# Performance work log

Hardware: AMD Instinct MI355X
Metric: run time of the kernel (lower is better)

The kernel has to match this reference:

```python
import jax, jax.numpy as jnp
import numpy as np

N_NODES = 100000
N_EDGES = 3200000
EMBED_DIM = 64
BATCH = 16384


def setup_inputs() -> dict:
    key = jax.random.key(0)
    k1, k2, k3, k4 = jax.random.split(key, 4)
    gcn_weight = jax.random.normal(k1, (N_NODES, EMBED_DIM), dtype=jnp.float32) * 0.1
    gcn_bias = jnp.zeros((EMBED_DIM,), dtype=jnp.float32)
    linear_weight = jax.random.normal(k2, (N_NODES, 1), dtype=jnp.float32) * 0.1
    linear_bias = jnp.zeros((1,), dtype=jnp.float32)
    edge_index = jax.random.randint(k3, (2, N_EDGES), 0, N_NODES, dtype=jnp.int64)
    interaction_pairs = jax.random.randint(k4, (BATCH, 2), 0, N_NODES, dtype=jnp.int64)
    return {
        "gcn_weight": gcn_weight,
        "gcn_bias": gcn_bias,
        "linear_weight": linear_weight,
        "linear_bias": linear_bias,
        "edge_index": edge_index,
        "interaction_pairs": interaction_pairs,
    }


def _gcn_conv_identity_features(gcn_weight, gcn_bias, edge_index):
    # Features X = I, so X @ W = W. GCNConv output = D^{-1/2}(A+I)D^{-1/2} W + b.
    src, dst = edge_index[0], edge_index[1]
    ones = jnp.ones((src.shape[0],), dtype=gcn_weight.dtype)
    # degree (with self loop) computed on destination nodes, as in PyG gcn_norm
    deg = jax.ops.segment_sum(ones, dst, num_segments=N_NODES) + 1.0
    dinv = jax.lax.rsqrt(deg)  # [N]
    norm = dinv[src] * dinv[dst]  # [E]
    msg = gcn_weight[src] * norm[:, None]  # [E, D] -- dominant memory traffic
    agg = jax.ops.segment_sum(msg, dst, num_segments=N_NODES)  # [N, D]
    # self-loop term: norm_ii = 1/deg[i]
    out = agg + gcn_weight * (dinv * dinv)[:, None] + gcn_bias
    return out


def reference(gcn_weight, gcn_bias, linear_weight, linear_bias, edge_index, interaction_pairs):
    node_emb = _gcn_conv_identity_features(gcn_weight, gcn_bias, edge_index)  # [N, D]
    e = node_emb[interaction_pairs]  # [B, 2, D] gather
    # FM pairwise interaction: 0.5 * sum_d ((sum_f e)^2 - sum_f e^2)
    sum_sq = jnp.square(jnp.sum(e, axis=1))  # [B, D]
    sq_sum = jnp.sum(jnp.square(e), axis=1)  # [B, D]
    fm = 0.5 * jnp.sum(sum_sq - sq_sum, axis=1, keepdims=True)  # [B, 1]
    # FeaturesLinear: sum of per-node scalar embeddings + bias
    lin = jnp.sum(linear_weight[interaction_pairs], axis=1) + linear_bias  # [B, 1]
    return jnp.squeeze(lin + fm, axis=1)  # [B]
```

## Files before the change

kernel.cpp:

```cpp
#include <hip/hip_runtime.h>

#define N_NODES 100000
#define N_EDGES 3200000
#define BATCH 16384
#define MAX_SLOTS 32768
#define MAGIC 0x5A5A5A5Au

#define NW 12500
#define SLICES 256
#define EPS2 12500
#define I4PS2 3125

#define NBUCK 256
#define BSH 7

#define OFF_SLOT      0
#define OFF_COUNTERS  400000
#define OFF_DINV      400064
#define OFF_NODELIST  800064
#define OFF_BTOT      931136
#define OFF_BPART     932160
#define OFF_SLOTSTART 1194304
#define OFF_PARTIALS  1325440
#define OFF_WH        14125440
#define OFF_BINS      26925440
#define OFF_BINS2     31725440
#define OFF_EMB       36525440

__device__ __forceinline__ unsigned bfr(float f) {
    unsigned u = __float_as_uint(f);
    return (u + 0x7FFFu + ((u >> 16) & 1u)) >> 16;
}
__device__ __forceinline__ float bfx(unsigned h) {
    return __uint_as_float(h << 16);
}

__global__ void k_flags(const int* __restrict__ pairs, unsigned* __restrict__ slot,
                        int* __restrict__ counters) {
    int i = blockIdx.x * blockDim.x + threadIdx.x;
    if (i < 16) counters[i] = 0;
    if (i < 2 * BATCH) slot[pairs[i]] = MAGIC;
}

__global__ void k_compact(unsigned* __restrict__ slot, int* __restrict__ nodelist,
                          int* __restrict__ counters) {
    int n = blockIdx.x * blockDim.x + threadIdx.x;
    int lane = threadIdx.x & 63;
    int want = (n < N_NODES && slot[n] == MAGIC) ? 1 : 0;
    int incl = want;
#pragma unroll
    for (int d = 1; d < 64; d <<= 1) {
        int t = __shfl_up(incl, d, 64);
        if (lane >= d) incl += t;
    }
    int total = __shfl(incl, 63, 64);
    int base = 0;
    if (lane == 63 && total > 0) base = atomicAdd(&counters[0], total);
    base = __shfl(base, 63, 64);
    if (n < N_NODES) {
        if (want) {
            int s = base + incl - 1;
            slot[n] = (unsigned)(s + 1);
            nodelist[s] = n;
        } else {
            slot[n] = 0u;
        }
    }
}

__device__ __forceinline__ void hist1n(int d, unsigned* h) {
    atomicAdd(&h[d >> 3], 1u << ((d & 7) << 2));
}

__global__ void k_hist(const int* __restrict__ dst, const unsigned* __restrict__ slot,
                       unsigned* __restrict__ partials, int* __restrict__ bpart) {
    __shared__ unsigned h[NW];
    __shared__ int lc[NBUCK];
    int g = blockIdx.x;
    for (int i = threadIdx.x; i < NW; i += 512) h[i] = 0;
    if (threadIdx.x < NBUCK) lc[threadIdx.x] = 0;
    __syncthreads();
    const int4* d4 = (const int4*)(dst + g * EPS2);
    for (int i = threadIdx.x; i < I4PS2; i += 512) {
        int4 v = d4[i];
        hist1n(v.x, h); hist1n(v.y, h); hist1n(v.z, h); hist1n(v.w, h);
        unsigned r;
        r = slot[v.x]; if (r) atomicAdd(&lc[(r - 1) >> BSH], 1);
        r = slot[v.y]; if (r) atomicAdd(&lc[(r - 1) >> BSH], 1);
        r = slot[v.z]; if (r) atomicAdd(&lc[(r - 1) >> BSH], 1);
        r = slot[v.w]; if (r) atomicAdd(&lc[(r - 1) >> BSH], 1);
    }
    __syncthreads();
    unsigned* outp = partials + (unsigned)g * NW;
    for (int i = threadIdx.x; i < NW; i += 512) outp[i] = h[i];
    if (threadIdx.x < NBUCK) bpart[threadIdx.x * SLICES + g] = lc[threadIdx.x];
}

__global__ void k_mid(const unsigned* __restrict__ partials, const float4* __restrict__ w4,
                      float* __restrict__ dinv, uint4* __restrict__ wh4,
                      int* __restrict__ bpart, int* __restrict__ btot) {
    if (blockIdx.x >= 391) {
        __shared__ int t[SLICES];
        int b = blockIdx.x - 391, g = threadIdx.x;
        int v = bpart[b * SLICES + g];
        t[g] = v;
        __syncthreads();
        for (int off = 1; off < SLICES; off <<= 1) {
            int x = (g >= off) ? t[g - off] : 0;
            __syncthreads();
            t[g] += x;
            __syncthreads();
        }
        bpart[b * SLICES + g] = t[g] - v;
        if (g == SLICES - 1) btot[b] = t[g];
        return;
    }
    __shared__ unsigned pA[256], pB[256], pC[256], pD[256];
    __shared__ float sdinv[256];
    int blk = blockIdx.x;
    int wi = threadIdx.x & 31, sg = threadIdx.x >> 5;
    int w = blk * 32 + wi;
    unsigned A = 0, B = 0, C = 0, D = 0;
    if (w < NW) {
        const unsigned* q = partials + w;
#pragma unroll
        for (int ch = 0; ch < 2; ++ch) {
            unsigned x = 0, y = 0;
#pragma unroll
            for (int k = 0; k < 16; ++k) {
                unsigned v = q[(unsigned)(sg * 32 + ch * 16 + k) * NW];
                x += v & 0x0F0F0F0Fu;
                y += (v >> 4) & 0x0F0F0F0Fu;
            }
            A += x & 0x00FF00FFu;
            B += (x >> 8) & 0x00FF00FFu;
            C += y & 0x00FF00FFu;
            D += (y >> 8) & 0x00FF00FFu;
        }
    }
    pA[threadIdx.x] = A; pB[threadIdx.x] = B; pC[threadIdx.x] = C; pD[threadIdx.x] = D;
    __syncthreads();
    if (threadIdx.x < 32 && w < NW) {
        unsigned sA = 0, sB = 0, sC = 0, sD = 0;
#pragma unroll
        for (int k = 0; k < 8; ++k) {
            sA += pA[k * 32 + wi]; sB += pB[k * 32 + wi];
            sC += pC[k * 32 + wi]; sD += pD[k * 32 + wi];
        }
        float4 d0, d1;
        d0.x = rsqrtf((float)(sA & 0xFFFFu) + 1.0f);
        d0.y = rsqrtf((float)(sC & 0xFFFFu) + 1.0f);
        d0.z = rsqrtf((float)(sB & 0xFFFFu) + 1.0f);
        d0.w = rsqrtf((float)(sD & 0xFFFFu) + 1.0f);
        d1.x = rsqrtf((float)(sA >> 16) + 1.0f);
        d1.y = rsqrtf((float)(sC >> 16) + 1.0f);
        d1.z = rsqrtf((float)(sB >> 16) + 1.0f);
        d1.w = rsqrtf((float)(sD >> 16) + 1.0f);
        ((float4*)dinv)[w * 2] = d0;
        ((float4*)dinv)[w * 2 + 1] = d1;
        int lb = wi * 8;
        sdinv[lb + 0] = d0.x; sdinv[lb + 1] = d0.y; sdinv[lb + 2] = d0.z; sdinv[lb + 3] = d0.w;
        sdinv[lb + 4] = d1.x; sdinv[lb + 5] = d1.y; sdinv[lb + 6] = d1.z; sdinv[lb + 7] = d1.w;
    }
    __syncthreads();
#pragma unroll
    for (int it = 0; it < 8; ++it) {
        int k = blk * 2048 + it * 256 + threadIdx.x;
        if (k < N_NODES * 8) {
            float4 va = w4[k * 2];
            float4 vb = w4[k * 2 + 1];
            float d = sdinv[(k >> 3) - blk * 256];
            uint4 o;
            o.x = bfr(va.x * d) | (bfr(va.y * d) << 16);
            o.y = bfr(va.z * d) | (bfr(va.w * d) << 16);
            o.z = bfr(vb.x * d) | (bfr(vb.y * d) << 16);
            o.w = bfr(vb.z * d) | (bfr(vb.w * d) << 16);
            wh4[k] = o;
        }
    }
}

__device__ __forceinline__ void scat1(int d, int s, const unsigned* __restrict__ slot,
                                      int* cur, int* __restrict__ bins) {
    unsigned r = slot[d];
    if (r) {
        int sl = (int)r - 1;
        int pos = atomicAdd(&cur[sl >> BSH], 1);
        bins[pos] = ((sl & 127) << 17) | s;
    }
}

__global__ void k_bscatter(const int* __restrict__ src, const int* __restrict__ dst,
                           const unsigned* __restrict__ slot, const int* __restrict__ bpart,
                           const int* __restrict__ btot, int* __restrict__ bins) {
    __shared__ int tb[NBUCK], vv[NBUCK], cur[NBUCK];
    int g = blockIdx.x;
    int t = threadIdx.x;
    if (t < NBUCK) { int v = btot[t]; vv[t] = v; tb[t] = v; }
    __syncthreads();
    for (int off = 1; off < NBUCK; off <<= 1) {
        int x = (t < NBUCK && t >= off) ? tb[t - off] : 0;
        __syncthreads();
        if (t < NBUCK) tb[t] += x;
        __syncthreads();
    }
    if (t < NBUCK) cur[t] = tb[t] - vv[t] + bpart[t * SLICES + g];
    __syncthreads();
    const int4* d4 = (const int4*)(dst + g * EPS2);
    const int4* s4 = (const int4*)(src + g * EPS2);
    for (int i = t; i < I4PS2; i += 512) {
        int4 d = d4[i];
        int4 s = s4[i];
        scat1(d.x, s.x, slot, cur, bins);
        scat1(d.y, s.y, slot, cur, bins);
        scat1(d.z, s.z, slot, cur, bins);
        scat1(d.w, s.w, slot, cur, bins);
    }
}

__global__ void k_bsort(const int* __restrict__ btot, const int* __restrict__ bins,
                        int* __restrict__ slotstart, int* __restrict__ bins2) {
    __shared__ int tb[NBUCK], vv[NBUCK];
    __shared__ int lc[128], st[128];
    int b = blockIdx.x;
    int tid = threadIdx.x;
    { int v = btot[tid]; vv[tid] = v; tb[tid] = v; }
    __syncthreads();
    for (int off = 1; off < NBUCK; off <<= 1) {
        int x = (tid >= off) ? tb[tid - off] : 0;
        __syncthreads();
        tb[tid] += x;
        __syncthreads();
    }
    int beg = tb[b] - vv[b];
    int end = beg + vv[b];
    if (tid < 128) lc[tid] = 0;
    __syncthreads();
    for (int j = beg + tid; j < end; j += 256)
        atomicAdd(&lc[(bins[j] >> 17) & 127], 1);
    __syncthreads();
    if (tid < 128) st[tid] = lc[tid];
    __syncthreads();
    for (int off = 1; off < 128; off <<= 1) {
        int v = (tid < 128 && tid >= off) ? st[tid - off] : 0;
        __syncthreads();
        if (tid < 128) st[tid] += v;
        __syncthreads();
    }
    if (tid < 128) {
        int s0 = beg + st[tid] - lc[tid];
        slotstart[(b << 7) + tid] = s0;
        lc[tid] = s0;
    }
    if (b == NBUCK - 1 && tid == 0) slotstart[MAX_SLOTS] = tb[NBUCK - 1];
    __syncthreads();
    for (int j = beg + tid; j < end; j += 256) {
        int e = bins[j];
        int pos = atomicAdd(&lc[(e >> 17) & 127], 1);
        bins2[pos] = e & 0x1FFFF;
    }
}

__global__ void k_gather(const int* __restrict__ nodelist, const int* __restrict__ slotstart,
                         const int* __restrict__ bins2, const uint4* __restrict__ wh4,
                         const float* __restrict__ dinv, const float4* __restrict__ bias4,
                         const int* __restrict__ counters, uint4* __restrict__ emb4) {
    int s = (blockIdx.x * blockDim.x + threadIdx.x) >> 6;
    int lane = threadIdx.x & 63;
    if (s >= counters[0]) return;
    int rg = lane >> 3, dp = lane & 7;
    int beg = slotstart[s], end = slotstart[s + 1];
    float a0 = 0.f, a1 = 0.f, a2 = 0.f, a3 = 0.f, a4 = 0.f, a5 = 0.f, a6 = 0.f, a7 = 0.f;
    int j = beg;
    for (; j + 16 <= end; j += 16) {
        int e0 = bins2[j + rg];
        int e1 = bins2[j + 8 + rg];
        uint4 oa = wh4[(e0 << 3) + dp];
        uint4 ob = wh4[(e1 << 3) + dp];
        a0 += bfx(oa.x) + bfx(ob.x);
        a1 += bfx(oa.x >> 16) + bfx(ob.x >> 16);
        a2 += bfx(oa.y) + bfx(ob.y);
        a3 += bfx(oa.y >> 16) + bfx(ob.y >> 16);
        a4 += bfx(oa.z) + bfx(ob.z);
        a5 += bfx(oa.z >> 16) + bfx(ob.z >> 16);
        a6 += bfx(oa.w) + bfx(ob.w);
        a7 += bfx(oa.w >> 16) + bfx(ob.w >> 16);
    }
    for (; j < end; j += 8) {
        if (rg < end - j) {
            int e0 = bins2[j + rg];
            uint4 oa = wh4[(e0 << 3) + dp];
            a0 += bfx(oa.x); a1 += bfx(oa.x >> 16);
            a2 += bfx(oa.y); a3 += bfx(oa.y >> 16);
            a4 += bfx(oa.z); a5 += bfx(oa.z >> 16);
            a6 += bfx(oa.w); a7 += bfx(oa.w >> 16);
        }
    }
#pragma unroll
    for (int m = 8; m <= 32; m <<= 1) {
        a0 += __shfl_xor(a0, m, 64); a1 += __shfl_xor(a1, m, 64);
        a2 += __shfl_xor(a2, m, 64); a3 += __shfl_xor(a3, m, 64);
        a4 += __shfl_xor(a4, m, 64); a5 += __shfl_xor(a5, m, 64);
        a6 += __shfl_xor(a6, m, 64); a7 += __shfl_xor(a7, m, 64);
    }
    if (rg == 0) {
        int n = nodelist[s];
        float dn = dinv[n];
        uint4 u = wh4[(n << 3) + dp];
        float4 b0 = bias4[dp * 2], b1 = bias4[dp * 2 + 1];
        float r0 = (a0 + bfx(u.x)) * dn + b0.x;
        float r1 = (a1 + bfx(u.x >> 16)) * dn + b0.y;
        float r2 = (a2 + bfx(u.y)) * dn + b0.z;
        float r3 = (a3 + bfx(u.y >> 16)) * dn + b0.w;
        float r4 = (a4 + bfx(u.z)) * dn + b1.x;
        float r5 = (a5 + bfx(u.z >> 16)) * dn + b1.y;
        float r6 = (a6 + bfx(u.w)) * dn + b1.z;
        float r7 = (a7 + bfx(u.w >> 16)) * dn + b1.w;
        uint4 o;
        o.x = bfr(r0) | (bfr(r1) << 16);
        o.y = bfr(r2) | (bfr(r3) << 16);
        o.z = bfr(r4) | (bfr(r5) << 16);
        o.w = bfr(r6) | (bfr(r7) << 16);
        emb4[(s << 3) + dp] = o;
    }
}

__global__ void k_final(const int* __restrict__ pairs, const unsigned* __restrict__ slot,
                        const uint2* __restrict__ emb2, const float* __restrict__ lw,
                        const float* __restrict__ lb, float* __restrict__ out) {
    int p = (blockIdx.x * blockDim.x + threadIdx.x) >> 4;
    int li = threadIdx.x & 15;
    if (p >= BATCH) return;
    int a = pairs[p * 2], b = pairs[p * 2 + 1];
    int sa = (int)slot[a] - 1;
    int sb = (int)slot[b] - 1;
    uint2 ua = emb2[(sa << 4) + li];
    uint2 ub = emb2[(sb << 4) + li];
    float prod = bfx(ua.x) * bfx(ub.x) + bfx(ua.x >> 16) * bfx(ub.x >> 16)
               + bfx(ua.y) * bfx(ub.y) + bfx(ua.y >> 16) * bfx(ub.y >> 16);
#pragma unroll
    for (int m = 1; m <= 8; m <<= 1) prod += __shfl_xor(prod, m, 64);
    if (li == 0) out[p] = lw[a] + lw[b] + lb[0] + prod;
}

extern "C" void kernel_launch(void* const* d_in, const int* in_sizes, int n_in,
                              void* d_out, int out_size, void* d_ws, size_t ws_size,
                              hipStream_t stream) {
    const float* gcn_weight    = (const float*)d_in[0];
    const float* gcn_bias      = (const float*)d_in[1];
    const float* linear_weight = (const float*)d_in[2];
    const float* linear_bias   = (const float*)d_in[3];
    const int*   edge_index    = (const int*)d_in[4];
    const int*   pairs         = (const int*)d_in[5];
    float* out = (float*)d_out;

    char* ws = (char*)d_ws;
    unsigned* slot      = (unsigned*)(ws + OFF_SLOT);
    int*      counters  = (int*)     (ws + OFF_COUNTERS);
    float*    dinv      = (float*)   (ws + OFF_DINV);
    int*      nodelist  = (int*)     (ws + OFF_NODELIST);
    int*      btot      = (int*)     (ws + OFF_BTOT);
    int*      bpart     = (int*)     (ws + OFF_BPART);
    int*      slotstart = (int*)     (ws + OFF_SLOTSTART);
    unsigned* partials  = (unsigned*)(ws + OFF_PARTIALS);
    uint4*    wh4       = (uint4*)   (ws + OFF_WH);
    int*      bins      = (int*)     (ws + OFF_BINS);
    int*      bins2     = (int*)     (ws + OFF_BINS2);
    uint4*    emb4      = (uint4*)   (ws + OFF_EMB);
    uint2*    emb2      = (uint2*)   (ws + OFF_EMB);

    const int* src_arr = edge_index;
    const int* dst_arr = edge_index + N_EDGES;

    k_flags<<<128, 256, 0, stream>>>(pairs, slot, counters);
    k_compact<<<391, 256, 0, stream>>>(slot, nodelist, counters);
    k_hist<<<SLICES, 512, 0, stream>>>(dst_arr, slot, partials, bpart);
    k_mid<<<391 + 256, 256, 0, stream>>>(partials, (const float4*)gcn_weight, dinv, wh4,
                                         bpart, btot);
    k_bscatter<<<SLICES, 512, 0, stream>>>(src_arr, dst_arr, slot, bpart, btot, bins);
    k_bsort<<<NBUCK, 256, 0, stream>>>(btot, bins, slotstart, bins2);
    k_gather<<<MAX_SLOTS / 4, 256, 0, stream>>>(nodelist, slotstart, bins2, wh4,
                                                dinv, (const float4*)gcn_bias,
                                                counters, emb4);
    k_final<<<1024, 256, 0, stream>>>(pairs, slot, emb2, linear_weight, linear_bias, out);
}
```

Baseline: 198.0 us.

## Fuse pipeline stages into one persistent kernel with software grid barriers

Replaces seven separate kernel launches with a single persistent 512-block kernel that runs compaction, histogram, dinv/bf16 conversion, prefix scans, bucket scatter, bucket sort, gather and final FM stages, separated by atomic-counter grid barriers. The bucket-partial granularity is doubled to 512 sub-slices so every block participates in the scatter phase. The aim is to remove per-launch overhead and inter-kernel gaps. In exchange it adds spin-wait barrier costs and depends on all 512 blocks being co-resident, which risks deadlock if occupancy is lower than assumed.

```diff
diff --git a/kernel.cpp b/kernel.cpp
--- a/kernel.cpp
+++ b/kernel.cpp
@@ -6,11 +6,12 @@
 #define MAX_SLOTS 32768
 #define MAGIC 0x5A5A5A5Au
 
+#define GRID 512
+#define TPB 512
+
 #define NW 12500
-#define SLICES 256
-#define EPS2 12500
-#define I4PS2 3125
-
+#define HSLICES 256
+#define NSUB 512
 #define NBUCK 256
 #define BSH 7
 
@@ -20,12 +21,12 @@
 #define OFF_NODELIST  800064
 #define OFF_BTOT      931136
 #define OFF_BPART     932160
-#define OFF_SLOTSTART 1194304
-#define OFF_PARTIALS  1325440
-#define OFF_WH        14125440
-#define OFF_BINS      26925440
-#define OFF_BINS2     31725440
-#define OFF_EMB       36525440
+#define OFF_SLOTSTART 1456448
+#define OFF_PARTIALS  1587584
+#define OFF_WH        14387584
+#define OFF_BINS      27187584
+#define OFF_BINS2     31987584
+#define OFF_EMB       36787584
 
 __device__ __forceinline__ unsigned bfr(float f) {
     unsigned u = __float_as_uint(f);
@@ -35,326 +36,29 @@
     return __uint_as_float(h << 16);
 }
 
-__global__ void k_flags(const int* __restrict__ pairs, unsigned* __restrict__ slot,
+__device__ __forceinline__ void gbar(int* cnt, int target) {
+    __syncthreads();
+    if (threadIdx.x == 0) {
+        __threadfence();
+        atomicAdd(cnt, 1);
+        while (atomicAdd(cnt, 0) < target) __builtin_amdgcn_s_sleep(8);
+        __threadfence();
+    }
+    __syncthreads();
+}
+
+__global__ void k_init0(const int* __restrict__ pairs, unsigned* __restrict__ slot,
                         int* __restrict__ counters) {
     int i = blockIdx.x * blockDim.x + threadIdx.x;
     if (i < 16) counters[i] = 0;
     if (i < 2 * BATCH) slot[pairs[i]] = MAGIC;
 }
 
-__global__ void k_compact(unsigned* __restrict__ slot, int* __restrict__ nodelist,
-                          int* __restrict__ counters) {
-    int n = blockIdx.x * blockDim.x + threadIdx.x;
-    int lane = threadIdx.x & 63;
-    int want = (n < N_NODES && slot[n] == MAGIC) ? 1 : 0;
-    int incl = want;
-#pragma unroll
-    for (int d = 1; d < 64; d <<= 1) {
-        int t = __shfl_up(incl, d, 64);
-        if (lane >= d) incl += t;
-    }
-    int total = __shfl(incl, 63, 64);
-    int base = 0;
-    if (lane == 63 && total > 0) base = atomicAdd(&counters[0], total);
-    base = __shfl(base, 63, 64);
-    if (n < N_NODES) {
-        if (want) {
-            int s = base + incl - 1;
-            slot[n] = (unsigned)(s + 1);
-            nodelist[s] = n;
-        } else {
-            slot[n] = 0u;
-        }
-    }
-}
-
-__device__ __forceinline__ void hist1n(int d, unsigned* h) {
-    atomicAdd(&h[d >> 3], 1u << ((d & 7) << 2));
-}
-
-__global__ void k_hist(const int* __restrict__ dst, const unsigned* __restrict__ slot,
-                       unsigned* __restrict__ partials, int* __restrict__ bpart) {
-    __shared__ unsigned h[NW];
-    __shared__ int lc[NBUCK];
-    int g = blockIdx.x;
-    for (int i = threadIdx.x; i < NW; i += 512) h[i] = 0;
-    if (threadIdx.x < NBUCK) lc[threadIdx.x] = 0;
-    __syncthreads();
-    const int4* d4 = (const int4*)(dst + g * EPS2);
-    for (int i = threadIdx.x; i < I4PS2; i += 512) {
-        int4 v = d4[i];
-        hist1n(v.x, h); hist1n(v.y, h); hist1n(v.z, h); hist1n(v.w, h);
-        unsigned r;
-        r = slot[v.x]; if (r) atomicAdd(&lc[(r - 1) >> BSH], 1);
-        r = slot[v.y]; if (r) atomicAdd(&lc[(r - 1) >> BSH], 1);
-        r = slot[v.z]; if (r) atomicAdd(&lc[(r - 1) >> BSH], 1);
-        r = slot[v.w]; if (r) atomicAdd(&lc[(r - 1) >> BSH], 1);
-    }
-    __syncthreads();
-    unsigned* outp = partials + (unsigned)g * NW;
-    for (int i = threadIdx.x; i < NW; i += 512) outp[i] = h[i];
-    if (threadIdx.x < NBUCK) bpart[threadIdx.x * SLICES + g] = lc[threadIdx.x];
-}
-
-__global__ void k_mid(const unsigned* __restrict__ partials, const float4* __restrict__ w4,
-                      float* __restrict__ dinv, uint4* __restrict__ wh4,
-                      int* __restrict__ bpart, int* __restrict__ btot) {
-    if (blockIdx.x >= 391) {
-        __shared__ int t[SLICES];
-        int b = blockIdx.x - 391, g = threadIdx.x;
-        int v = bpart[b * SLICES + g];
-        t[g] = v;
-        __syncthreads();
-        for (int off = 1; off < SLICES; off <<= 1) {
-            int x = (g >= off) ? t[g - off] : 0;
-            __syncthreads();
-            t[g] += x;
-            __syncthreads();
-        }
-        bpart[b * SLICES + g] = t[g] - v;
-        if (g == SLICES - 1) btot[b] = t[g];
-        return;
-    }
-    __shared__ unsigned pA[256], pB[256], pC[256], pD[256];
-    __shared__ float sdinv[256];
-    int blk = blockIdx.x;
-    int wi = threadIdx.x & 31, sg = threadIdx.x >> 5;
-    int w = blk * 32 + wi;
-    unsigned A = 0, B = 0, C = 0, D = 0;
-    if (w < NW) {
-        const unsigned* q = partials + w;
-#pragma unroll
-        for (int ch = 0; ch < 2; ++ch) {
-            unsigned x = 0, y = 0;
-#pragma unroll
-            for (int k = 0; k < 16; ++k) {
-                unsigned v = q[(unsigned)(sg * 32 + ch * 16 + k) * NW];
-                x += v & 0x0F0F0F0Fu;
-                y += (v >> 4) & 0x0F0F0F0Fu;
-            }
-            A += x & 0x00FF00FFu;
-            B += (x >> 8) & 0x00FF00FFu;
-            C += y & 0x00FF00FFu;
-            D += (y >> 8) & 0x00FF00FFu;
-        }
-    }
-    pA[threadIdx.x] = A; pB[threadIdx.x] = B; pC[threadIdx.x] = C; pD[threadIdx.x] = D;
-    __syncthreads();
-    if (threadIdx.x < 32 && w < NW) {
-        unsigned sA = 0, sB = 0, sC = 0, sD = 0;
-#pragma unroll
-        for (int k = 0; k < 8; ++k) {
-            sA += pA[k * 32 + wi]; sB += pB[k * 32 + wi];
-            sC += pC[k * 32 + wi]; sD += pD[k * 32 + wi];
-        }
-        float4 d0, d1;
-        d0.x = rsqrtf((float)(sA & 0xFFFFu) + 1.0f);
-        d0.y = rsqrtf((float)(sC & 0xFFFFu) + 1.0f);
-        d0.z = rsqrtf((float)(sB & 0xFFFFu) + 1.0f);
-        d0.w = rsqrtf((float)(sD & 0xFFFFu) + 1.0f);
-        d1.x = rsqrtf((float)(sA >> 16) + 1.0f);
-        d1.y = rsqrtf((float)(sC >> 16) + 1.0f);
-        d1.z = rsqrtf((float)(sB >> 16) + 1.0f);
-        d1.w = rsqrtf((float)(sD >> 16) + 1.0f);
-        ((float4*)dinv)[w * 2] = d0;
-        ((float4*)dinv)[w * 2 + 1] = d1;
-        int lb = wi * 8;
-        sdinv[lb + 0] = d0.x; sdinv[lb + 1] = d0.y; sdinv[lb + 2] = d0.z; sdinv[lb + 3] = d0.w;
-        sdinv[lb + 4] = d1.x; sdinv[lb + 5] = d1.y; sdinv[lb + 6] = d1.z; sdinv[lb + 7] = d1.w;
-    }
-    __syncthreads();
-#pragma unroll
-    for (int it = 0; it < 8; ++it) {
-        int k = blk * 2048 + it * 256 + threadIdx.x;
-        if (k < N_NODES * 8) {
-            float4 va = w4[k * 2];
-            float4 vb = w4[k * 2 + 1];
-            float d = sdinv[(k >> 3) - blk * 256];
-            uint4 o;
-            o.x = bfr(va.x * d) | (bfr(va.y * d) << 16);
-            o.y = bfr(va.z * d) | (bfr(va.w * d) << 16);
-            o.z = bfr(vb.x * d) | (bfr(vb.y * d) << 16);
-            o.w = bfr(vb.z * d) | (bfr(vb.w * d) << 16);
-            wh4[k] = o;
-        }
-    }
-}
-
-__device__ __forceinline__ void scat1(int d, int s, const unsigned* __restrict__ slot,
-                                      int* cur, int* __restrict__ bins) {
-    unsigned r = slot[d];
-    if (r) {
-        int sl = (int)r - 1;
-        int pos = atomicAdd(&cur[sl >> BSH], 1);
-        bins[pos] = ((sl & 127) << 17) | s;
-    }
-}
-
-__global__ void k_bscatter(const int* __restrict__ src, const int* __restrict__ dst,
-                           const unsigned* __restrict__ slot, const int* __restrict__ bpart,
-                           const int* __restrict__ btot, int* __restrict__ bins) {
-    __shared__ int tb[NBUCK], vv[NBUCK], cur[NBUCK];
-    int g = blockIdx.x;
-    int t = threadIdx.x;
-    if (t < NBUCK) { int v = btot[t]; vv[t] = v; tb[t] = v; }
-    __syncthreads();
-    for (int off = 1; off < NBUCK; off <<= 1) {
-        int x = (t < NBUCK && t >= off) ? tb[t - off] : 0;
-        __syncthreads();
-        if (t < NBUCK) tb[t] += x;
-        __syncthreads();
-    }
-    if (t < NBUCK) cur[t] = tb[t] - vv[t] + bpart[t * SLICES + g];
-    __syncthreads();
-    const int4* d4 = (const int4*)(dst + g * EPS2);
-    const int4* s4 = (const int4*)(src + g * EPS2);
-    for (int i = t; i < I4PS2; i += 512) {
-        int4 d = d4[i];
-        int4 s = s4[i];
-        scat1(d.x, s.x, slot, cur, bins);
-        scat1(d.y, s.y, slot, cur, bins);
-        scat1(d.z, s.z, slot, cur, bins);
-        scat1(d.w, s.w, slot, cur, bins);
-    }
-}
-
-__global__ void k_bsort(const int* __restrict__ btot, const int* __restrict__ bins,
-                        int* __restrict__ slotstart, int* __restrict__ bins2) {
-    __shared__ int tb[NBUCK], vv[NBUCK];
-    __shared__ int lc[128], st[128];
-    int b = blockIdx.x;
-    int tid = threadIdx.x;
-    { int v = btot[tid]; vv[tid] = v; tb[tid] = v; }
-    __syncthreads();
-    for (int off = 1; off < NBUCK; off <<= 1) {
-        int x = (tid >= off) ? tb[tid - off] : 0;
-        __syncthreads();
-        tb[tid] += x;
-        __syncthreads();
-    }
-    int beg = tb[b] - vv[b];
-    int end = beg + vv[b];
-    if (tid < 128) lc[tid] = 0;
-    __syncthreads();
-    for (int j = beg + tid; j < end; j += 256)
-        atomicAdd(&lc[(bins[j] >> 17) & 127], 1);
-    __syncthreads();
-    if (tid < 128) st[tid] = lc[tid];
-    __syncthreads();
-    for (int off = 1; off < 128; off <<= 1) {
-        int v = (tid < 128 && tid >= off) ? st[tid - off] : 0;
-        __syncthreads();
-        if (tid < 128) st[tid] += v;
-        __syncthreads();
-    }
-    if (tid < 128) {
-        int s0 = beg + st[tid] - lc[tid];
-        slotstart[(b << 7) + tid] = s0;
-        lc[tid] = s0;
-    }
-    if (b == NBUCK - 1 && tid == 0) slotstart[MAX_SLOTS] = tb[NBUCK - 1];
-    __syncthreads();
-    for (int j = beg + tid; j < end; j += 256) {
-        int e = bins[j];
-        int pos = atomicAdd(&lc[(e >> 17) & 127], 1);
-        bins2[pos] = e & 0x1FFFF;
-    }
-}
-
-__global__ void k_gather(const int* __restrict__ nodelist, const int* __restrict__ slotstart,
-                         const int* __restrict__ bins2, const uint4* __restrict__ wh4,
-                         const float* __restrict__ dinv, const float4* __restrict__ bias4,
-                         const int* __restrict__ counters, uint4* __restrict__ emb4) {
-    int s = (blockIdx.x * blockDim.x + threadIdx.x) >> 6;
-    int lane = threadIdx.x & 63;
-    if (s >= counters[0]) return;
-    int rg = lane >> 3, dp = lane & 7;
-    int beg = slotstart[s], end = slotstart[s + 1];
-    float a0 = 0.f, a1 = 0.f, a2 = 0.f, a3 = 0.f, a4 = 0.f, a5 = 0.f, a6 = 0.f, a7 = 0.f;
-    int j = beg;
-    for (; j + 16 <= end; j += 16) {
-        int e0 = bins2[j + rg];
-        int e1 = bins2[j + 8 + rg];
-        uint4 oa = wh4[(e0 << 3) + dp];
-        uint4 ob = wh4[(e1 << 3) + dp];
-        a0 += bfx(oa.x) + bfx(ob.x);
-        a1 += bfx(oa.x >> 16) + bfx(ob.x >> 16);
-        a2 += bfx(oa.y) + bfx(ob.y);
-        a3 += bfx(oa.y >> 16) + bfx(ob.y >> 16);
-        a4 += bfx(oa.z) + bfx(ob.z);
-        a5 += bfx(oa.z >> 16) + bfx(ob.z >> 16);
-        a6 += bfx(oa.w) + bfx(ob.w);
-        a7 += bfx(oa.w >> 16) + bfx(ob.w >> 16);
-    }
-    for (; j < end; j += 8) {
-        if (rg < end - j) {
-            int e0 = bins2[j + rg];
-            uint4 oa = wh4[(e0 << 3) + dp];
-            a0 += bfx(oa.x); a1 += bfx(oa.x >> 16);
-            a2 += bfx(oa.y); a3 += bfx(oa.y >> 16);
-            a4 += bfx(oa.z); a5 += bfx(oa.z >> 16);
-            a6 += bfx(oa.w); a7 += bfx(oa.w >> 16);
-        }
-    }
-#pragma unroll
-    for (int m = 8; m <= 32; m <<= 1) {
-        a0 += __shfl_xor(a0, m, 64); a1 += __shfl_xor(a1, m, 64);
-        a2 += __shfl_xor(a2, m, 64); a3 += __shfl_xor(a3, m, 64);
-        a4 += __shfl_xor(a4, m, 64); a5 += __shfl_xor(a5, m, 64);
-        a6 += __shfl_xor(a6, m, 64); a7 += __shfl_xor(a7, m, 64);
-    }
-    if (rg == 0) {
-        int n = nodelist[s];
-        float dn = dinv[n];
-        uint4 u = wh4[(n << 3) + dp];
-        float4 b0 = bias4[dp * 2], b1 = bias4[dp * 2 + 1];
-        float r0 = (a0 + bfx(u.x)) * dn + b0.x;
-        float r1 = (a1 + bfx(u.x >> 16)) * dn + b0.y;
-        float r2 = (a2 + bfx(u.y)) * dn + b0.z;
-        float r3 = (a3 + bfx(u.y >> 16)) * dn + b0.w;
-        float r4 = (a4 + bfx(u.z)) * dn + b1.x;
-        float r5 = (a5 + bfx(u.z >> 16)) * dn + b1.y;
-        float r6 = (a6 + bfx(u.w)) * dn + b1.z;
-        float r7 = (a7 + bfx(u.w >> 16)) * dn + b1.w;
-        uint4 o;
-        o.x = bfr(r0) | (bfr(r1) << 16);
-        o.y = bfr(r2) | (bfr(r3) << 16);
-        o.z = bfr(r4) | (bfr(r5) << 16);
-        o.w = bfr(r6) | (bfr(r7) << 16);
-        emb4[(s << 3) + dp] = o;
-    }
-}
-
-__global__ void k_final(const int* __restrict__ pairs, const unsigned* __restrict__ slot,
-                        const uint2* __restrict__ emb2, const float* __restrict__ lw,
-                        const float* __restrict__ lb, float* __restrict__ out) {
-    int p = (blockIdx.x * blockDim.x + threadIdx.x) >> 4;
-    int li = threadIdx.x & 15;
-    if (p >= BATCH) return;
-    int a = pairs[p * 2], b = pairs[p * 2 + 1];
-    int sa = (int)slot[a] - 1;
-    int sb = (int)slot[b] - 1;
-    uint2 ua = emb2[(sa << 4) + li];
-    uint2 ub = emb2[(sb << 4) + li];
-    float prod = bfx(ua.x) * bfx(ub.x) + bfx(ua.x >> 16) * bfx(ub.x >> 16)
-               + bfx(ua.y) * bfx(ub.y) + bfx(ua.y >> 16) * bfx(ub.y >> 16);
-#pragma unroll
-    for (int m = 1; m <= 8; m <<= 1) prod += __shfl_xor(prod, m, 64);
-    if (li == 0) out[p] = lw[a] + lw[b] + lb[0] + prod;
-}
-
-extern "C" void kernel_launch(void* const* d_in, const int* in_sizes, int n_in,
-                              void* d_out, int out_size, void* d_ws, size_t ws_size,
-                              hipStream_t stream) {
-    const float* gcn_weight    = (const float*)d_in[0];
-    const float* gcn_bias      = (const float*)d_in[1];
-    const float* linear_weight = (const float*)d_in[2];
-    const float* linear_bias   = (const float*)d_in[3];
-    const int*   edge_index    = (const int*)d_in[4];
-    const int*   pairs         = (const int*)d_in[5];
-    float* out = (float*)d_out;
-
-    char* ws = (char*)d_ws;
+__global__ __launch_bounds__(TPB, 4) void k_mega(
+        const float4* __restrict__ w4, const float4* __restrict__ bias4,
+        const float* __restrict__ lw, const float* __restrict__ lb,
+        const int* __restrict__ src, const int* __restrict__ dst,
+        const int* __restrict__ pairs, float* __restrict__ out, char* __restrict__ ws) {
     unsigned* slot      = (unsigned*)(ws + OFF_SLOT);
     int*      counters  = (int*)     (ws + OFF_COUNTERS);
     float*    dinv      = (float*)   (ws + OFF_DINV);
@@ -367,20 +71,328 @@
     int*      bins      = (int*)     (ws + OFF_BINS);
     int*      bins2     = (int*)     (ws + OFF_BINS2);
     uint4*    emb4      = (uint4*)   (ws + OFF_EMB);
-    uint2*    emb2      = (uint2*)   (ws + OFF_EMB);
+    const uint2* emb2   = (const uint2*)(ws + OFF_EMB);
+    int* cnt = &counters[1];
+
+    __shared__ union SM {
+        struct { unsigned h[NW]; int lc[2][NBUCK]; } c;
+        struct { unsigned p[4][TPB]; float sdinv[256]; } d;
+        struct { int t[NSUB]; } pfx;
+        struct { int tb[NBUCK], vv[NBUCK], cur[NBUCK]; } e;
+        struct { int tb[NBUCK], vv[NBUCK], lc[128], st[128]; } f;
+    } sm;
+
+    int tid = threadIdx.x;
+
+    {
+        int n = blockIdx.x * TPB + tid;
+        int lane = tid & 63;
+        int want = (n < N_NODES && slot[n] == MAGIC) ? 1 : 0;
+        int incl = want;
+#pragma unroll
+        for (int d = 1; d < 64; d <<= 1) {
+            int t = __shfl_up(incl, d, 64);
+            if (lane >= d) incl += t;
+        }
+        int total = __shfl(incl, 63, 64);
+        int base = 0;
+        if (lane == 63 && total > 0) base = atomicAdd(&counters[0], total);
+        base = __shfl(base, 63, 64);
+        if (n < N_NODES) {
+            if (want) {
+                int s = base + incl - 1;
+                slot[n] = (unsigned)(s + 1);
+                nodelist[s] = n;
+            } else {
+                slot[n] = 0u;
+            }
+        }
+    }
+    gbar(cnt, GRID);
+
+    if (blockIdx.x < HSLICES) {
+        int g = blockIdx.x;
+        for (int i = tid; i < NW; i += TPB) sm.c.h[i] = 0;
+        if (tid < NBUCK) { sm.c.lc[0][tid] = 0; sm.c.lc[1][tid] = 0; }
+        __syncthreads();
+        const int4* d4 = (const int4*)(dst + g * 12500);
+        for (int i = tid; i < 3125; i += TPB) {
+            int4 v = d4[i];
+            atomicAdd(&sm.c.h[v.x >> 3], 1u << ((v.x & 7) << 2));
+            atomicAdd(&sm.c.h[v.y >> 3], 1u << ((v.y & 7) << 2));
+            atomicAdd(&sm.c.h[v.z >> 3], 1u << ((v.z & 7) << 2));
+            atomicAdd(&sm.c.h[v.w >> 3], 1u << ((v.w & 7) << 2));
+            int s01 = (i * 4) >= 6250;
+            int s23 = (i * 4 + 2) >= 6250;
+            unsigned r;
+            r = slot[v.x]; if (r) atomicAdd(&sm.c.lc[s01][(r - 1) >> BSH], 1);
+            r = slot[v.y]; if (r) atomicAdd(&sm.c.lc[s01][(r - 1) >> BSH], 1);
+            r = slot[v.z]; if (r) atomicAdd(&sm.c.lc[s23][(r - 1) >> BSH], 1);
+            r = slot[v.w]; if (r) atomicAdd(&sm.c.lc[s23][(r - 1) >> BSH], 1);
+        }
+        __syncthreads();
+        unsigned* outp = partials + (unsigned)g * NW;
+        for (int i = tid; i < NW; i += TPB) outp[i] = sm.c.h[i];
+        if (tid < NBUCK) {
+            bpart[tid * NSUB + g * 2]     = sm.c.lc[0][tid];
+            bpart[tid * NSUB + g * 2 + 1] = sm.c.lc[1][tid];
+        }
+    }
+    gbar(cnt, 2 * GRID);
+
+    if (blockIdx.x < 391) {
+        int wi = tid & 31, sg = tid >> 5;
+        int w = blockIdx.x * 32 + wi;
+        unsigned A = 0, Bu = 0, Cu = 0, Du = 0;
+        if (w < NW) {
+            const unsigned* q = partials + w;
+            unsigned x = 0, y = 0;
+#pragma unroll
+            for (int k = 0; k < 16; ++k) {
+                unsigned v = q[(unsigned)(sg * 16 + k) * NW];
+                x += v & 0x0F0F0F0Fu;
+                y += (v >> 4) & 0x0F0F0F0Fu;
+            }
+            A = x & 0x00FF00FFu; Bu = (x >> 8) & 0x00FF00FFu;
+            Cu = y & 0x00FF00FFu; Du = (y >> 8) & 0x00FF00FFu;
+        }
+        sm.d.p[0][tid] = A; sm.d.p[1][tid] = Bu; sm.d.p[2][tid] = Cu; sm.d.p[3][tid] = Du;
+        __syncthreads();
+        if (tid < 32 && w < NW) {
+            unsigned sA = 0, sB = 0, sC = 0, sD = 0;
+#pragma unroll
+            for (int k = 0; k < 16; ++k) {
+                sA += sm.d.p[0][k * 32 + tid]; sB += sm.d.p[1][k * 32 + tid];
+                sC += sm.d.p[2][k * 32 + tid]; sD += sm.d.p[3][k * 32 + tid];
+            }
+            float4 d0, d1;
+            d0.x = rsqrtf((float)(sA & 0xFFFFu) + 1.0f);
+            d0.y = rsqrtf((float)(sC & 0xFFFFu) + 1.0f);
+            d0.z = rsqrtf((float)(sB & 0xFFFFu) + 1.0f);
+            d0.w = rsqrtf((float)(sD & 0xFFFFu) + 1.0f);
+            d1.x = rsqrtf((float)(sA >> 16) + 1.0f);
+            d1.y = rsqrtf((float)(sC >> 16) + 1.0f);
+            d1.z = rsqrtf((float)(sB >> 16) + 1.0f);
+            d1.w = rsqrtf((float)(sD >> 16) + 1.0f);
+            ((float4*)dinv)[w * 2] = d0;
+            ((float4*)dinv)[w * 2 + 1] = d1;
+            int lbm = tid * 8;
+            sm.d.sdinv[lbm + 0] = d0.x; sm.d.sdinv[lbm + 1] = d0.y;
+            sm.d.sdinv[lbm + 2] = d0.z; sm.d.sdinv[lbm + 3] = d0.w;
+            sm.d.sdinv[lbm + 4] = d1.x; sm.d.sdinv[lbm + 5] = d1.y;
+            sm.d.sdinv[lbm + 6] = d1.z; sm.d.sdinv[lbm + 7] = d1.w;
+        }
+        __syncthreads();
+#pragma unroll
+        for (int it = 0; it < 4; ++it) {
+            int k = blockIdx.x * 2048 + it * TPB + tid;
+            if (k < N_NODES * 8) {
+                float4 va = w4[k * 2];
+                float4 vb = w4[k * 2 + 1];
+                float d = sm.d.sdinv[(k >> 3) - blockIdx.x * 256];
+                uint4 o;
+                o.x = bfr(va.x * d) | (bfr(va.y * d) << 16);
+                o.y = bfr(va.z * d) | (bfr(va.w * d) << 16);
+                o.z = bfr(vb.x * d) | (bfr(vb.y * d) << 16);
+                o.w = bfr(vb.z * d) | (bfr(vb.w * d) << 16);
+                wh4[k] = o;
+            }
+        }
+    } else {
+        for (int r = blockIdx.x - 391; r < NBUCK; r += 121) {
+            int v = bpart[r * NSUB + tid];
+            sm.pfx.t[tid] = v;
+            __syncthreads();
+            for (int off = 1; off < NSUB; off <<= 1) {
+                int x = (tid >= off) ? sm.pfx.t[tid - off] : 0;
+                __syncthreads();
+                sm.pfx.t[tid] += x;
+                __syncthreads();
+            }
+            bpart[r * NSUB + tid] = sm.pfx.t[tid] - v;
+            if (tid == NSUB - 1) btot[r] = sm.pfx.t[tid];
+            __syncthreads();
+        }
+    }
+    gbar(cnt, 3 * GRID);
+
+    {
+        int u = blockIdx.x;
+        if (tid < NBUCK) { int v = btot[tid]; sm.e.vv[tid] = v; sm.e.tb[tid] = v; }
+        __syncthreads();
+        for (int off = 1; off < NBUCK; off <<= 1) {
+            int x = (tid < NBUCK && tid >= off) ? sm.e.tb[tid - off] : 0;
+            __syncthreads();
+            if (tid < NBUCK) sm.e.tb[tid] += x;
+            __syncthreads();
+        }
+        if (tid < NBUCK) sm.e.cur[tid] = sm.e.tb[tid] - sm.e.vv[tid] + bpart[tid * NSUB + u];
+        __syncthreads();
+        const int2* d2 = (const int2*)(dst + u * 6250);
+        const int2* s2 = (const int2*)(src + u * 6250);
+        for (int i = tid; i < 3125; i += TPB) {
+            int2 d = d2[i];
+            int2 s = s2[i];
+            unsigned r;
+            r = slot[d.x];
+            if (r) {
+                int sl = (int)r - 1;
+                int pos = atomicAdd(&sm.e.cur[sl >> BSH], 1);
+                bins[pos] = ((sl & 127) << 17) | s.x;
+            }
+            r = slot[d.y];
+            if (r) {
+                int sl = (int)r - 1;
+                int pos = atomicAdd(&sm.e.cur[sl >> BSH], 1);
+                bins[pos] = ((sl & 127) << 17) | s.y;
+            }
+        }
+    }
+    gbar(cnt, 4 * GRID);
+
+    if (blockIdx.x < NBUCK) {
+        int b = blockIdx.x;
+        if (tid < NBUCK) { int v = btot[tid]; sm.f.vv[tid] = v; sm.f.tb[tid] = v; }
+        __syncthreads();
+        for (int off = 1; off < NBUCK; off <<= 1) {
+            int x = (tid < NBUCK && tid >= off) ? sm.f.tb[tid - off] : 0;
+            __syncthreads();
+            if (tid < NBUCK) sm.f.tb[tid] += x;
+            __syncthreads();
+        }
+        int beg = sm.f.tb[b] - sm.f.vv[b];
+        int end = beg + sm.f.vv[b];
+        if (tid < 128) sm.f.lc[tid] = 0;
+        __syncthreads();
+        for (int j = beg + tid; j < end; j += TPB)
+            atomicAdd(&sm.f.lc[(bins[j] >> 17) & 127], 1);
+        __syncthreads();
+        if (tid < 128) sm.f.st[tid] = sm.f.lc[tid];
+        __syncthreads();
+        for (int off = 1; off < 128; off <<= 1) {
+            int v = (tid < 128 && tid >= off) ? sm.f.st[tid - off] : 0;
+            __syncthreads();
+            if (tid < 128) sm.f.st[tid] += v;
+            __syncthreads();
+        }
+        if (tid < 128) {
+            int s0 = beg + sm.f.st[tid] - sm.f.lc[tid];
+            slotstart[(b << 7) + tid] = s0;
+            sm.f.lc[tid] = s0;
+        }
+        if (b == NBUCK - 1 && tid == 0) slotstart[MAX_SLOTS] = sm.f.tb[NBUCK - 1];
+        __syncthreads();
+        for (int j = beg + tid; j < end; j += TPB) {
+            int e = bins[j];
+            int pos = atomicAdd(&sm.f.lc[(e >> 17) & 127], 1);
+            bins2[pos] = e & 0x1FFFF;
+        }
+    }
+    gbar(cnt, 5 * GRID);
+
+    {
+        int nS = counters[0];
+        int wv = blockIdx.x * (TPB / 64) + (tid >> 6);
+        int lane = tid & 63;
+        int rg = lane >> 3, dp = lane & 7;
+        for (int s = wv; s < nS; s += GRID * (TPB / 64)) {
+            int beg = slotstart[s], end = slotstart[s + 1];
+            float a0 = 0.f, a1 = 0.f, a2 = 0.f, a3 = 0.f,
+                  a4 = 0.f, a5 = 0.f, a6 = 0.f, a7 = 0.f;
+            int j = beg;
+            for (; j + 16 <= end; j += 16) {
+                int e0 = bins2[j + rg];
+                int e1 = bins2[j + 8 + rg];
+                uint4 oa = wh4[(e0 << 3) + dp];
+                uint4 ob = wh4[(e1 << 3) + dp];
+                a0 += bfx(oa.x) + bfx(ob.x);
+                a1 += bfx(oa.x >> 16) + bfx(ob.x >> 16);
+                a2 += bfx(oa.y) + bfx(ob.y);
+                a3 += bfx(oa.y >> 16) + bfx(ob.y >> 16);
+                a4 += bfx(oa.z) + bfx(ob.z);
+                a5 += bfx(oa.z >> 16) + bfx(ob.z >> 16);
+                a6 += bfx(oa.w) + bfx(ob.w);
+                a7 += bfx(oa.w >> 16) + bfx(ob.w >> 16);
+            }
+            for (; j < end; j += 8) {
+                if (rg < end - j) {
+                    int e0 = bins2[j + rg];
+                    uint4 oa = wh4[(e0 << 3) + dp];
+                    a0 += bfx(oa.x); a1 += bfx(oa.x >> 16);
+                    a2 += bfx(oa.y); a3 += bfx(oa.y >> 16);
+                    a4 += bfx(oa.z); a5 += bfx(oa.z >> 16);
+                    a6 += bfx(oa.w); a7 += bfx(oa.w >> 16);
+                }
+            }
+#pragma unroll
+            for (int m = 8; m <= 32; m <<= 1) {
+                a0 += __shfl_xor(a0, m, 64); a1 += __shfl_xor(a1, m, 64);
+                a2 += __shfl_xor(a2, m, 64); a3 += __shfl_xor(a3, m, 64);
+                a4 += __shfl_xor(a4, m, 64); a5 += __shfl_xor(a5, m, 64);
+                a6 += __shfl_xor(a6, m, 64); a7 += __shfl_xor(a7, m, 64);
+            }
+            if (rg == 0) {
+                int n = nodelist[s];
+                float dn = dinv[n];
+                uint4 u = wh4[(n << 3) + dp];
+                float4 b0 = bias4[dp * 2], b1 = bias4[dp * 2 + 1];
+                float r0 = (a0 + bfx(u.x)) * dn + b0.x;
+                float r1 = (a1 + bfx(u.x >> 16)) * dn + b0.y;
+                float r2 = (a2 + bfx(u.y)) * dn + b0.z;
+                float r3 = (a3 + bfx(u.y >> 16)) * dn + b0.w;
+                float r4 = (a4 + bfx(u.z)) * dn + b1.x;
+                float r5 = (a5 + bfx(u.z >> 16)) * dn + b1.y;
+                float r6 = (a6 + bfx(u.w)) * dn + b1.z;
+                float r7 = (a7 + bfx(u.w >> 16)) * dn + b1.w;
+                uint4 o;
+                o.x = bfr(r0) | (bfr(r1) << 16);
+                o.y = bfr(r2) | (bfr(r3) << 16);
+                o.z = bfr(r4) | (bfr(r5) << 16);
+                o.w = bfr(r6) | (bfr(r7) << 16);
+                emb4[(s << 3) + dp] = o;
+            }
+        }
+    }
+    gbar(cnt, 6 * GRID);
+
+    {
+        int p = (blockIdx.x * TPB + tid) >> 4;
+        int li = tid & 15;
+        if (p < BATCH) {
+            int a = pairs[p * 2], b = pairs[p * 2 + 1];
+            int sa = (int)slot[a] - 1;
+            int sb = (int)slot[b] - 1;
+            uint2 ua = emb2[(sa << 4) + li];
+            uint2 ub = emb2[(sb << 4) + li];
+            float prod = bfx(ua.x) * bfx(ub.x) + bfx(ua.x >> 16) * bfx(ub.x >> 16)
+                       + bfx(ua.y) * bfx(ub.y) + bfx(ua.y >> 16) * bfx(ub.y >> 16);
+#pragma unroll
+            for (int m = 1; m <= 8; m <<= 1) prod += __shfl_xor(prod, m, 64);
+            if (li == 0) out[p] = lw[a] + lw[b] + lb[0] + prod;
+        }
+    }
+}
+
+extern "C" void kernel_launch(void* const* d_in, const int* in_sizes, int n_in,
+                              void* d_out, int out_size, void* d_ws, size_t ws_size,
+                              hipStream_t stream) {
+    const float* gcn_weight    = (const float*)d_in[0];
+    const float* gcn_bias      = (const float*)d_in[1];
+    const float* linear_weight = (const float*)d_in[2];
+    const float* linear_bias   = (const float*)d_in[3];
+    const int*   edge_index    = (const int*)d_in[4];
+    const int*   pairs         = (const int*)d_in[5];
+    float* out = (float*)d_out;
+
+    char* ws = (char*)d_ws;
+    unsigned* slot     = (unsigned*)(ws + OFF_SLOT);
+    int*      counters = (int*)     (ws + OFF_COUNTERS);
 
     const int* src_arr = edge_index;
     const int* dst_arr = edge_index + N_EDGES;
 
-    k_flags<<<128, 256, 0, stream>>>(pairs, slot, counters);
-    k_compact<<<391, 256, 0, stream>>>(slot, nodelist, counters);
-    k_hist<<<SLICES, 512, 0, stream>>>(dst_arr, slot, partials, bpart);
-    k_mid<<<391 + 256, 256, 0, stream>>>(partials, (const float4*)gcn_weight, dinv, wh4,
-                                         bpart, btot);
-    k_bscatter<<<SLICES, 512, 0, stream>>>(src_arr, dst_arr, slot, bpart, btot, bins);
-    k_bsort<<<NBUCK, 256, 0, stream>>>(btot, bins, slotstart, bins2);
-    k_gather<<<MAX_SLOTS / 4, 256, 0, stream>>>(nodelist, slotstart, bins2, wh4,
-                                                dinv, (const float4*)gcn_bias,
-                                                counters, emb4);
-    k_final<<<1024, 256, 0, stream>>>(pairs, slot, emb2, linear_weight, linear_bias, out);
-}
+    k_init0<<<128, 256, 0, stream>>>(pairs, slot, counters);
+    k_mega<<<GRID, TPB, 0, stream>>>((const float4*)gcn_weight, (const float4*)gcn_bias,
+                                     linear_weight, linear_bias, src_arr, dst_arr,
+                                     pairs, out, ws);
+}
```

Result: slower. 514.0 us (+159.7%).

## Replace flag+compact passes with certified slot lookup via nodelist back-check

Applied to the files above, without the earlier changes.

The separate compaction kernel and its global counter go away. Each pair index now writes its own position into slot and nodelist, and a slot entry is treated as valid only if nodelist points back to the node. This avoids clearing slot across calls and removes one launch plus a full scan of all nodes. In exchange, every edge lookup in hist and scatter does an extra dependent nodelist read, and gather always processes all 32768 slots, including duplicate-pair slots that receive no edges.

```diff
diff --git a/kernel.cpp b/kernel.cpp
--- a/kernel.cpp
+++ b/kernel.cpp
@@ -4,7 +4,6 @@
 #define N_EDGES 3200000
 #define BATCH 16384
 #define MAX_SLOTS 32768
-#define MAGIC 0x5A5A5A5Au
 
 #define NW 12500
 #define SLICES 256
@@ -15,7 +14,6 @@
 #define BSH 7
 
 #define OFF_SLOT      0
-#define OFF_COUNTERS  400000
 #define OFF_DINV      400064
 #define OFF_NODELIST  800064
 #define OFF_BTOT      931136
@@ -36,43 +34,25 @@
 }
 
 __global__ void k_flags(const int* __restrict__ pairs, unsigned* __restrict__ slot,
-                        int* __restrict__ counters) {
+                        int* __restrict__ nodelist) {
     int i = blockIdx.x * blockDim.x + threadIdx.x;
-    if (i < 16) counters[i] = 0;
-    if (i < 2 * BATCH) slot[pairs[i]] = MAGIC;
-}
-
-__global__ void k_compact(unsigned* __restrict__ slot, int* __restrict__ nodelist,
-                          int* __restrict__ counters) {
-    int n = blockIdx.x * blockDim.x + threadIdx.x;
-    int lane = threadIdx.x & 63;
-    int want = (n < N_NODES && slot[n] == MAGIC) ? 1 : 0;
-    int incl = want;
-#pragma unroll
-    for (int d = 1; d < 64; d <<= 1) {
-        int t = __shfl_up(incl, d, 64);
-        if (lane >= d) incl += t;
-    }
-    int total = __shfl(incl, 63, 64);
-    int base = 0;
-    if (lane == 63 && total > 0) base = atomicAdd(&counters[0], total);
-    base = __shfl(base, 63, 64);
-    if (n < N_NODES) {
-        if (want) {
-            int s = base + incl - 1;
-            slot[n] = (unsigned)(s + 1);
-            nodelist[s] = n;
-        } else {
-            slot[n] = 0u;
-        }
-    }
-}
-
-__device__ __forceinline__ void hist1n(int d, unsigned* h) {
-    atomicAdd(&h[d >> 3], 1u << ((d & 7) << 2));
+    if (i < 2 * BATCH) {
+        int n = pairs[i];
+        nodelist[i] = n;
+        slot[n] = (unsigned)(i + 1);
+    }
+}
+
+__device__ __forceinline__ int cert(int d, const unsigned* __restrict__ slot,
+                                    const int* __restrict__ nodelist) {
+    unsigned r = slot[d];
+    unsigned idx = r - 1u;
+    if (idx < (unsigned)MAX_SLOTS && nodelist[idx] == d) return (int)idx;
+    return -1;
 }
 
 __global__ void k_hist(const int* __restrict__ dst, const unsigned* __restrict__ slot,
+                       const int* __restrict__ nodelist,
                        unsigned* __restrict__ partials, int* __restrict__ bpart) {
     __shared__ unsigned h[NW];
     __shared__ int lc[NBUCK];
@@ -83,12 +63,15 @@
     const int4* d4 = (const int4*)(dst + g * EPS2);
     for (int i = threadIdx.x; i < I4PS2; i += 512) {
         int4 v = d4[i];
-        hist1n(v.x, h); hist1n(v.y, h); hist1n(v.z, h); hist1n(v.w, h);
-        unsigned r;
-        r = slot[v.x]; if (r) atomicAdd(&lc[(r - 1) >> BSH], 1);
-        r = slot[v.y]; if (r) atomicAdd(&lc[(r - 1) >> BSH], 1);
-        r = slot[v.z]; if (r) atomicAdd(&lc[(r - 1) >> BSH], 1);
-        r = slot[v.w]; if (r) atomicAdd(&lc[(r - 1) >> BSH], 1);
+        atomicAdd(&h[v.x >> 3], 1u << ((v.x & 7) << 2));
+        atomicAdd(&h[v.y >> 3], 1u << ((v.y & 7) << 2));
+        atomicAdd(&h[v.z >> 3], 1u << ((v.z & 7) << 2));
+        atomicAdd(&h[v.w >> 3], 1u << ((v.w & 7) << 2));
+        int t;
+        t = cert(v.x, slot, nodelist); if (t >= 0) atomicAdd(&lc[t >> BSH], 1);
+        t = cert(v.y, slot, nodelist); if (t >= 0) atomicAdd(&lc[t >> BSH], 1);
+        t = cert(v.z, slot, nodelist); if (t >= 0) atomicAdd(&lc[t >> BSH], 1);
+        t = cert(v.w, slot, nodelist); if (t >= 0) atomicAdd(&lc[t >> BSH], 1);
     }
     __syncthreads();
     unsigned* outp = partials + (unsigned)g * NW;
@@ -180,19 +163,10 @@
     }
 }
 
-__device__ __forceinline__ void scat1(int d, int s, const unsigned* __restrict__ slot,
-                                      int* cur, int* __restrict__ bins) {
-    unsigned r = slot[d];
-    if (r) {
-        int sl = (int)r - 1;
-        int pos = atomicAdd(&cur[sl >> BSH], 1);
-        bins[pos] = ((sl & 127) << 17) | s;
-    }
-}
-
 __global__ void k_bscatter(const int* __restrict__ src, const int* __restrict__ dst,
-                           const unsigned* __restrict__ slot, const int* __restrict__ bpart,
-                           const int* __restrict__ btot, int* __restrict__ bins) {
+                           const unsigned* __restrict__ slot, const int* __restrict__ nodelist,
+                           const int* __restrict__ bpart, const int* __restrict__ btot,
+                           int* __restrict__ bins) {
     __shared__ int tb[NBUCK], vv[NBUCK], cur[NBUCK];
     int g = blockIdx.x;
     int t = threadIdx.x;
@@ -211,10 +185,15 @@
     for (int i = t; i < I4PS2; i += 512) {
         int4 d = d4[i];
         int4 s = s4[i];
-        scat1(d.x, s.x, slot, cur, bins);
-        scat1(d.y, s.y, slot, cur, bins);
-        scat1(d.z, s.z, slot, cur, bins);
-        scat1(d.w, s.w, slot, cur, bins);
+        int sl;
+        sl = cert(d.x, slot, nodelist);
+        if (sl >= 0) { int pos = atomicAdd(&cur[sl >> BSH], 1); bins[pos] = ((sl & 127) << 17) | s.x; }
+        sl = cert(d.y, slot, nodelist);
+        if (sl >= 0) { int pos = atomicAdd(&cur[sl >> BSH], 1); bins[pos] = ((sl & 127) << 17) | s.y; }
+        sl = cert(d.z, slot, nodelist);
+        if (sl >= 0) { int pos = atomicAdd(&cur[sl >> BSH], 1); bins[pos] = ((sl & 127) << 17) | s.z; }
+        sl = cert(d.w, slot, nodelist);
+        if (sl >= 0) { int pos = atomicAdd(&cur[sl >> BSH], 1); bins[pos] = ((sl & 127) << 17) | s.w; }
     }
 }
 
@@ -264,10 +243,9 @@
 __global__ void k_gather(const int* __restrict__ nodelist, const int* __restrict__ slotstart,
                          const int* __restrict__ bins2, const uint4* __restrict__ wh4,
                          const float* __restrict__ dinv, const float4* __restrict__ bias4,
-                         const int* __restrict__ counters, uint4* __restrict__ emb4) {
+                         uint4* __restrict__ emb4) {
     int s = (blockIdx.x * blockDim.x + threadIdx.x) >> 6;
     int lane = threadIdx.x & 63;
-    if (s >= counters[0]) return;
     int rg = lane >> 3, dp = lane & 7;
     int beg = slotstart[s], end = slotstart[s + 1];
     float a0 = 0.f, a1 = 0.f, a2 = 0.f, a3 = 0.f, a4 = 0.f, a5 = 0.f, a6 = 0.f, a7 = 0.f;
@@ -356,7 +334,6 @@
 
     char* ws = (char*)d_ws;
     unsigned* slot      = (unsigned*)(ws + OFF_SLOT);
-    int*      counters  = (int*)     (ws + OFF_COUNTERS);
     float*    dinv      = (float*)   (ws + OFF_DINV);
     int*      nodelist  = (int*)     (ws + OFF_NODELIST);
     int*      btot      = (int*)     (ws + OFF_BTOT);
@@ -372,15 +349,13 @@
     const int* src_arr = edge_index;
     const int* dst_arr = edge_index + N_EDGES;
 
-    k_flags<<<128, 256, 0, stream>>>(pairs, slot, counters);
-    k_compact<<<391, 256, 0, stream>>>(slot, nodelist, counters);
-    k_hist<<<SLICES, 512, 0, stream>>>(dst_arr, slot, partials, bpart);
+    k_flags<<<128, 256, 0, stream>>>(pairs, slot, nodelist);
+    k_hist<<<SLICES, 512, 0, stream>>>(dst_arr, slot, nodelist, partials, bpart);
     k_mid<<<391 + 256, 256, 0, stream>>>(partials, (const float4*)gcn_weight, dinv, wh4,
                                          bpart, btot);
-    k_bscatter<<<SLICES, 512, 0, stream>>>(src_arr, dst_arr, slot, bpart, btot, bins);
+    k_bscatter<<<SLICES, 512, 0, stream>>>(src_arr, dst_arr, slot, nodelist, bpart, btot, bins);
     k_bsort<<<NBUCK, 256, 0, stream>>>(btot, bins, slotstart, bins2);
     k_gather<<<MAX_SLOTS / 4, 256, 0, stream>>>(nodelist, slotstart, bins2, wh4,
-                                                dinv, (const float4*)gcn_bias,
-                                                counters, emb4);
+                                                dinv, (const float4*)gcn_bias, emb4);
     k_final<<<1024, 256, 0, stream>>>(pairs, slot, emb2, linear_weight, linear_bias, out);
 }
```

New measurement: 191.7 us. 3.2% less time.
